# Optimization experiments

Hardware: AMD Instinct MI355X
Metric: run time of the kernel (lower is better)

## Reference

```python
import jax, jax.numpy as jnp
import numpy as np
import math

B, L, D, H, FF = 2, 2048, 1024, 16, 4096
FACTOR = 5
EPS = 1e-5


def _ln(x, g, b):
    mu = jnp.mean(x, axis=-1, keepdims=True)
    var = jnp.mean((x - mu) ** 2, axis=-1, keepdims=True)
    return (x - mu) * jax.lax.rsqrt(var + EPS) * g + b


def setup_inputs() -> dict:
    key = jax.random.key(0)
    ks = jax.random.split(key, 16)
    s = D ** -0.5
    sample_k = min(FACTOR * int(np.ceil(np.log(L))), L)  # 40
    return {
        "x": jax.random.normal(ks[0], (B, L, D), jnp.float32),
        "Wq": jax.random.normal(ks[1], (D, D), jnp.float32) * s,
        "bq": jnp.zeros((D,), jnp.float32),
        "Wk": jax.random.normal(ks[2], (D, D), jnp.float32) * s,
        "bk": jnp.zeros((D,), jnp.float32),
        "Wv": jax.random.normal(ks[3], (D, D), jnp.float32) * s,
        "bv": jnp.zeros((D,), jnp.float32),
        "Wo": jax.random.normal(ks[4], (D, D), jnp.float32) * s,
        "bo": jnp.zeros((D,), jnp.float32),
        "ln1_g": jnp.ones((D,), jnp.float32),
        "ln1_b": jnp.zeros((D,), jnp.float32),
        "W1": jax.random.normal(ks[5], (D, FF), jnp.float32) * s,
        "b1": jnp.zeros((FF,), jnp.float32),
        "W2": jax.random.normal(ks[6], (FF, D), jnp.float32) * (FF ** -0.5),
        "b2": jnp.zeros((D,), jnp.float32),
        "ln2_g": jnp.ones((D,), jnp.float32),
        "ln2_b": jnp.zeros((D,), jnp.float32),
        "index_sample": jax.random.randint(ks[7], (L, sample_k), 0, L),
    }


def _prob_attn(Q, K, V, index_sample):
    # Q,K,V: [B,H,L,Dh]; Informer ProbAttention with mask_flag=True (causal).
    b, h, l, dh = Q.shape
    n_top = min(FACTOR * int(np.ceil(np.log(l))), l)
    # sampled scores: Q[l] . K[index_sample[l, s]]
    K_s = K[:, :, index_sample]                                  # [B,H,L,S,Dh]
    QKs = jnp.einsum("bhld,bhlsd->bhls", Q, K_s)                 # [B,H,L,S]
    M = QKs.max(-1) - QKs.sum(-1) / l                             # sparsity measure
    _, M_top = jax.lax.top_k(M, n_top)                            # [B,H,u]
    Q_red = jnp.take_along_axis(Q, M_top[..., None], axis=2)      # [B,H,u,Dh]
    scale = 1.0 / jnp.sqrt(jnp.asarray(dh, jnp.float32))
    scores = jnp.einsum("bhud,bhld->bhul", Q_red, K) * scale      # [B,H,u,L]
    causal = jnp.arange(l)[None, None, None, :] > M_top[..., None]
    scores = jnp.where(causal, -jnp.inf, scores)
    attn = jax.nn.softmax(scores, axis=-1)
    upd = jnp.einsum("bhul,bhld->bhud", attn, V)                  # [B,H,u,Dh]
    # initial context for masked case: running cumsum of V
    context = jnp.cumsum(V, axis=2)
    bi = jnp.arange(b)[:, None, None]
    hi = jnp.arange(h)[None, :, None]
    context = context.at[bi, hi, M_top].set(upd)
    return context                                               # [B,H,L,Dh]


def reference(x, Wq, bq, Wk, bk, Wv, bv, Wo, bo, ln1_g, ln1_b,
              W1, b1, W2, b2, ln2_g, ln2_b, index_sample):
    b, l, d = x.shape
    dh = d // H
    Q = (x @ Wq + bq).reshape(b, l, H, dh).transpose(0, 2, 1, 3)
    K = (x @ Wk + bk).reshape(b, l, H, dh).transpose(0, 2, 1, 3)
    V = (x @ Wv + bv).reshape(b, l, H, dh).transpose(0, 2, 1, 3)
    ctx = _prob_attn(Q, K, V, index_sample)
    ctx = ctx.transpose(0, 2, 1, 3).reshape(b, l, d)
    attn_out = ctx @ Wo + bo
    x1 = _ln(x + attn_out, ln1_g, ln1_b)
    ff = jnp.maximum(x1 @ W1 + b1, 0.0) @ W2 + b2
    return _ln(x1 + ff, ln2_g, ln2_b)
```

## Files before the change

kernel.cpp:

```cpp
#include <hip/hip_runtime.h>
#include <hip/hip_bf16.h>
#include <hip/hip_fp16.h>
#include <math.h>

constexpr int B = 2, L = 2048, D = 1024, H = 16, DH = 64, FFD = 4096;
constexpr int S = 40;
constexpr int U = 40;
constexpr float EPS = 1e-5f;
constexpr int NCHUNK = 32;
constexpr int CHLEN = L / NCHUNK;
constexpr int LD3 = 3 * D;
constexpr int LD2 = 2 * D;
constexpr int LDA2 = 2 * D;
constexpr int JT = 128;
constexpr int NJC = L / JT;

typedef __attribute__((ext_vector_type(8))) short short8;
typedef __attribute__((ext_vector_type(8))) _Float16 half8;
typedef __attribute__((ext_vector_type(4))) float f32x4;

__device__ __forceinline__ unsigned short f2bf(float v) {
  __hip_bfloat16 h = __float2bfloat16(v);
  return __builtin_bit_cast(unsigned short, h);
}
__device__ __forceinline__ float bf2f(unsigned short u) {
  unsigned int x = ((unsigned int)u) << 16;
  return __builtin_bit_cast(float, x);
}
__device__ __forceinline__ unsigned short f2h(float v) {
  __half h = __float2half(v);
  return __builtin_bit_cast(unsigned short, h);
}
__device__ __forceinline__ float h2f(unsigned short u) {
  return __half2float(__builtin_bit_cast(__half, u));
}

__device__ __forceinline__ void gload16(const void* g, void* l) {
  __builtin_amdgcn_global_load_lds(
      (const __attribute__((address_space(1))) void*)g,
      (__attribute__((address_space(3))) void*)l, 16, 0, 0);
}

template<int GBN, int MINB, bool RELU, bool OUT_BF16, bool F16, bool DUPA>
__global__ __launch_bounds__(256, MINB) void gemm_kernel(
    const unsigned short* __restrict__ A,
    const unsigned short* __restrict__ Bt,
    const float* __restrict__ bias,
    const float* __restrict__ biasB,
    void* __restrict__ C, int M, int N, int K, int KA) {
  constexpr int GBM = 128, GBK = 64;
  constexpr int ABUF = GBM * GBK;
  constexpr int BBUF = GBN * GBK;
  constexpr int BUFS = ABUF + BBUF;
  constexpr int NI = GBN / 32;
  constexpr int NLOADS = 4 + GBN / 32;
  __shared__ short lds[2 * BUFS];

  const int tid  = threadIdx.x;
  const int lane = tid & 63;
  const int wid  = tid >> 6;
  const int wr = wid >> 1;
  const int wc = wid & 1;

  const int nwg  = gridDim.x * gridDim.y;
  const int orig = blockIdx.y * gridDim.x + blockIdx.x;
  const int wg   = (orig & 7) * (nwg >> 3) + (orig >> 3);
  const int bm = (wg / gridDim.x) * GBM;
  const int bn = (wg % gridDim.x) * GBN;

  const int srow  = lane >> 3;
  const int sslot = (lane & 7) ^ srow;
  const unsigned short* aS = A  + (size_t)(bm + wid * 8 + srow) * KA + sslot * 8;
  const unsigned short* bS = Bt + (size_t)(bn + wid * 8 + srow) * K  + sslot * 8;
  short* la0 = lds + wid * 8 * GBK;
  short* lb0 = lds + ABUF + wid * 8 * GBK;

  auto STAGE = [&](int buf, int kt) {
    const int akt = (DUPA && kt >= 16) ? kt - 16 : kt;
    const unsigned short* ap = aS + (size_t)akt * GBK;
    const unsigned short* bp = bS + (size_t)kt  * GBK;
    short* la = la0 + buf * BUFS;
    short* lb = lb0 + buf * BUFS;
    gload16(ap,                   la);
    gload16(ap + (size_t)32 * KA, la + 32 * GBK);
    gload16(ap + (size_t)64 * KA, la + 64 * GBK);
    gload16(ap + (size_t)96 * KA, la + 96 * GBK);
    #pragma unroll
    for (int r = 0; r < GBN / 32; ++r)
      gload16(bp + (size_t)(r * 32) * K, lb + r * 32 * GBK);
  };

  const int fr = lane & 15, g = lane >> 4;
  const int nt = K / GBK;

  STAGE(0, 0);

  f32x4 acc[4][NI] = {};
  int cur = 0;
  for (int t = 0; t < nt; ++t) {
    const int kt = (t + 1 < nt) ? t + 1 : t;
    STAGE(cur ^ 1, kt);
    if constexpr (NLOADS == 8)
      asm volatile("s_waitcnt vmcnt(8)" ::: "memory");
    else
      asm volatile("s_waitcnt vmcnt(6)" ::: "memory");
    __builtin_amdgcn_sched_barrier(0);
    __builtin_amdgcn_s_barrier();

    const short* la = lds + cur * BUFS;
    const short* lb = la + ABUF;
    short8 av[2][4], bv[2][NI];
    #pragma unroll
    for (int kk = 0; kk < 2; ++kk) {
      #pragma unroll
      for (int mi = 0; mi < 4; ++mi) {
        const int row = wr * 64 + mi * 16 + fr;
        av[kk][mi] = *(const short8*)&la[row * GBK + ((((kk << 2) | g) ^ (fr & 7)) << 3)];
      }
      #pragma unroll
      for (int ni = 0; ni < NI; ++ni) {
        const int row = wc * (GBN / 2) + ni * 16 + fr;
        bv[kk][ni] = *(const short8*)&lb[row * GBK + ((((kk << 2) | g) ^ (fr & 7)) << 3)];
      }
    }
    __builtin_amdgcn_s_setprio(1);
    #pragma unroll
    for (int kk = 0; kk < 2; ++kk)
      #pragma unroll
      for (int mi = 0; mi < 4; ++mi)
        #pragma unroll
        for (int ni = 0; ni < NI; ++ni) {
          if constexpr (F16)
            acc[mi][ni] = __builtin_amdgcn_mfma_f32_16x16x32_f16(
                __builtin_bit_cast(half8, av[kk][mi]),
                __builtin_bit_cast(half8, bv[kk][ni]), acc[mi][ni], 0, 0, 0);
          else
            acc[mi][ni] = __builtin_amdgcn_mfma_f32_16x16x32_bf16(
                av[kk][mi], bv[kk][ni], acc[mi][ni], 0, 0, 0);
        }
    __builtin_amdgcn_s_setprio(0);
    asm volatile("s_waitcnt lgkmcnt(0)" ::: "memory");
    __builtin_amdgcn_sched_barrier(0);
    __builtin_amdgcn_s_barrier();
    cur ^= 1;
  }

  #pragma unroll
  for (int ni = 0; ni < NI; ++ni) {
    const int col = bn + wc * (GBN / 2) + ni * 16 + fr;
    const float bcol = DUPA ? (col < D ? bias[col] : biasB[col - D]) : bias[col];
    #pragma unroll
    for (int mi = 0; mi < 4; ++mi) {
      #pragma unroll
      for (int j = 0; j < 4; ++j) {
        const int rowg = bm + wr * 64 + mi * 16 + (g << 2) + j;
        float v = acc[mi][ni][j] + bcol;
        if (RELU) v = fmaxf(v, 0.f);
        if (OUT_BF16) ((unsigned short*)C)[(size_t)rowg * N + col] = f2bf(v);
        else          ((float*)C)[(size_t)rowg * N + col] = v;
      }
    }
  }
}

__global__ __launch_bounds__(256) void split_x_f16_kernel(
    const float* __restrict__ x, unsigned short* __restrict__ A2,
    unsigned short* __restrict__ xb) {
  const int i = (blockIdx.x * 256 + threadIdx.x) * 4;
  if (i >= B * L * D) return;
  const int m = i / D, k = i % D;
  const float4 v = *(const float4*)(x + i);
  ushort4 hi, lo, bb;
  hi.x = f2h(v.x); lo.x = f2h(v.x - h2f(hi.x)); bb.x = f2bf(v.x);
  hi.y = f2h(v.y); lo.y = f2h(v.y - h2f(hi.y)); bb.y = f2bf(v.y);
  hi.z = f2h(v.z); lo.z = f2h(v.z - h2f(hi.z)); bb.z = f2bf(v.z);
  hi.w = f2h(v.w); lo.w = f2h(v.w - h2f(hi.w)); bb.w = f2bf(v.w);
  unsigned short* row = A2 + (size_t)m * LDA2;
  *(ushort4*)(row + k)     = hi;
  *(ushort4*)(row + D + k) = lo;
  *(ushort4*)(xb + i) = bb;
}

__global__ __launch_bounds__(256) void wsplit_f16_kernel(
    const float* __restrict__ W, unsigned short* __restrict__ B2r) {
  __shared__ float tile[32][33];
  const int bx = blockIdx.x * 32;
  const int by = blockIdx.y * 32;
  const int tx = threadIdx.x & 31, ty = threadIdx.x >> 5;
  #pragma unroll
  for (int i = ty; i < 32; i += 8)
    tile[i][tx] = W[(size_t)(by + i) * D + bx + tx];
  __syncthreads();
  #pragma unroll
  for (int i = ty; i < 32; i += 8) {
    const float v = tile[tx][i];
    const unsigned short hi = f2h(v);
    const unsigned short lo = f2h(v - h2f(hi));
    unsigned short* r = B2r + (size_t)(bx + i) * LD3 + (by + tx);
    r[0]     = hi;
    r[D]     = lo;
    r[2 * D] = hi;
  }
}

__global__ __launch_bounds__(256) void transpose4_bf16_kernel(
    const float* __restrict__ Wv, const float* __restrict__ Wo,
    const float* __restrict__ W1, const float* __restrict__ W2,
    unsigned short* __restrict__ Wvt, unsigned short* __restrict__ Wot,
    unsigned short* __restrict__ W1t, unsigned short* __restrict__ W2t) {
  const int bid = blockIdx.x;
  const float* W; unsigned short* Wt; int K, N, t;
  if (bid < 1024)      { W = Wv; Wt = Wvt; K = D;   N = D;   t = bid; }
  else if (bid < 2048) { W = Wo; Wt = Wot; K = D;   N = D;   t = bid - 1024; }
  else if (bid < 6144) { W = W1; Wt = W1t; K = D;   N = FFD; t = bid - 2048; }
  else                 { W = W2; Wt = W2t; K = FFD; N = D;   t = bid - 6144; }
  const int nx = N / 32;
  const int bx = (t % nx) * 32;
  const int by = (t / nx) * 32;
  __shared__ float tile[32][33];
  const int tx = threadIdx.x & 31, ty = threadIdx.x >> 5;
  #pragma unroll
  for (int i = ty; i < 32; i += 8)
    tile[i][tx] = W[(size_t)(by + i) * N + bx + tx];
  __syncthreads();
  #pragma unroll
  for (int i = ty; i < 32; i += 8)
    Wt[(size_t)(bx + i) * K + by + tx] = f2bf(tile[tx][i]);
}

__global__ __launch_bounds__(256) void prob_m_kernel(
    const float* __restrict__ QK, const int* __restrict__ idx,
    float* __restrict__ M_) {
  const int combo = blockIdx.x;
  const int b = combo >> 2, hg = combo & 3;
  const int l = blockIdx.y;
  const int tid = threadIdx.x;
  const int wave = tid >> 6;
  const int lane = tid & 63;
  const int h = hg * 4 + wave;
  __shared__ int sidx[S];
  if (tid < S) sidx[tid] = idx[l * S + tid];
  __syncthreads();
  const int dsub = (lane & 15) * 4;
  const int sgrp = lane >> 4;
  const float4 q = *(const float4*)(QK + ((size_t)b * L + l) * LD2 + h * DH + dsub);
  float mx = -INFINITY, sm = 0.f;
  for (int s = sgrp; s < S; s += 4) {
    const float4 kv = *(const float4*)(QK + ((size_t)b * L + sidx[s]) * LD2 + D + h * DH + dsub);
    float p = q.x*kv.x + q.y*kv.y + q.z*kv.z + q.w*kv.w;
    p += __shfl_xor(p, 1);
    p += __shfl_xor(p, 2);
    p += __shfl_xor(p, 4);
    p += __shfl_xor(p, 8);
    mx = fmaxf(mx, p);
    sm += p;
  }
  mx = fmaxf(mx, __shfl_xor(mx, 16));
  mx = fmaxf(mx, __shfl_xor(mx, 32));
  sm += __shfl_xor(sm, 16);
  sm += __shfl_xor(sm, 32);
  if (lane == 0)
    M_[((size_t)b * H + h) * L + l] = mx - sm / (float)L;
}

__global__ __launch_bounds__(64) void topk_kernel(
    const float* __restrict__ M_, int* __restrict__ Mtop) {
  const int bh = blockIdx.x;
  const float* row = M_ + (size_t)bh * L;
  const int lane = threadIdx.x;
  float v[32];
  #pragma unroll
  for (int k = 0; k < 32; ++k) v[k] = row[k * 64 + lane];
  for (int u = 0; u < U; ++u) {
    float best = v[0]; int bk = 0;
    #pragma unroll
    for (int k = 1; k < 32; ++k)
      if (v[k] > best) { best = v[k]; bk = k; }
    int bidx = bk * 64 + lane;
    #pragma unroll
    for (int off = 1; off < 64; off <<= 1) {
      const float ov = __shfl_xor(best, off);
      const int   oi = __shfl_xor(bidx, off);
      if (ov > best || (ov == best && oi < bidx)) { best = ov; bidx = oi; }
    }
    if (lane == 0) Mtop[bh * U + u] = bidx;
    if ((bidx & 63) == lane) {
      const int kk = bidx >> 6;
      #pragma unroll
      for (int k = 0; k < 32; ++k) if (k == kk) v[k] = -INFINITY;
    }
  }
}

__global__ __launch_bounds__(320) void attn_p1_kernel(
    const float* __restrict__ QK, const float* __restrict__ V,
    const int* __restrict__ Mtop,
    float* __restrict__ pmax, float* __restrict__ psum, float* __restrict__ pv) {
  const int jc = blockIdx.x, h = blockIdx.y, b = blockIdx.z;
  const int bh = b * H + h;
  const int tid = threadIdx.x;
  const int j0 = jc * JT;
  __shared__ float Qs[U][68];
  __shared__ float KVs[JT][68];
  __shared__ unsigned short ws[U][JT];

  for (int i = tid; i < U * 16; i += 320) {
    const int u = i >> 4, dq = (i & 15) << 2;
    const int row = Mtop[bh * U + u];
    *(float4*)&Qs[u][dq] =
        *(const float4*)(QK + ((size_t)b * L + row) * LD2 + h * DH + dq);
  }
  for (int i = tid; i < JT * 16; i += 320) {
    const int j = i >> 4, dq = (i & 15) << 2;
    *(float4*)&KVs[j][dq] =
        *(const float4*)(QK + ((size_t)b * L + j0 + j) * LD2 + D + h * DH + dq);
  }
  __syncthreads();

  const int u = tid >> 3, jg = tid & 7;
  const int mt = Mtop[bh * U + u];
  float sc[16];
  #pragma unroll
  for (int jt = 0; jt < 16; ++jt) sc[jt] = 0.f;
  for (int dq = 0; dq < 64; dq += 4) {
    const float4 q = *(const float4*)&Qs[u][dq];
    #pragma unroll
    for (int jt = 0; jt < 16; ++jt) {
      const float4 k = *(const float4*)&KVs[jt * 8 + jg][dq];
      sc[jt] += q.x*k.x + q.y*k.y + q.z*k.z + q.w*k.w;
    }
  }
  float m = -INFINITY;
  #pragma unroll
  for (int jt = 0; jt < 16; ++jt) {
    const int j = j0 + jt * 8 + jg;
    sc[jt] = (j <= mt) ? sc[jt] * 0.125f : -INFINITY;
    m = fmaxf(m, sc[jt]);
  }
  m = fmaxf(m, __shfl_xor(m, 1));
  m = fmaxf(m, __shfl_xor(m, 2));
  m = fmaxf(m, __shfl_xor(m, 4));
  float sum = 0.f;
  #pragma unroll
  for (int jt = 0; jt < 16; ++jt) {
    const float e = (sc[jt] == -INFINITY) ? 0.f : expf(sc[jt] - m);
    sum += e;
    ws[u][jt * 8 + jg] = f2bf(e);
  }
  sum += __shfl_xor(sum, 1);
  sum += __shfl_xor(sum, 2);
  sum += __shfl_xor(sum, 4);
  if (jg == 0) {
    pmax[(size_t)(bh * NJC + jc) * U + u] = m;
    psum[(size_t)(bh * NJC + jc) * U + u] = sum;
  }
  __syncthreads();
  for (int i = tid; i < JT * 16; i += 320) {
    const int j = i >> 4, dq = (i & 15) << 2;
    *(float4*)&KVs[j][dq] =
        *(const float4*)(V + ((size_t)b * L + j0 + j) * D + h * DH + dq);
  }
  __syncthreads();
  const int d = tid & 63, ug = tid >> 6;
  float acc[8] = {};
  for (int j = 0; j < JT; j += 2) {
    const float v0 = KVs[j][d], v1 = KVs[j + 1][d];
    #pragma unroll
    for (int k = 0; k < 8; ++k) {
      const int uu = ug + k * 5;
      const unsigned int wp = *(const unsigned int*)&ws[uu][j];
      acc[k] = fmaf(bf2f((unsigned short)(wp & 0xffff)), v0, acc[k]);
      acc[k] = fmaf(bf2f((unsigned short)(wp >> 16)), v1, acc[k]);
    }
  }
  #pragma unroll
  for (int k = 0; k < 8; ++k) {
    const int uu = ug + k * 5;
    pv[((size_t)(bh * NJC + jc) * U + uu) * DH + d] = acc[k];
  }
}

__global__ __launch_bounds__(64) void attn_p2_kernel(
    const float* __restrict__ pmax, const float* __restrict__ psum,
    const float* __restrict__ pv, const int* __restrict__ Mtop,
    unsigned short* __restrict__ ctx16) {
  const int bid = blockIdx.x;
  const int u = bid % U, bh = bid / U;
  const int d = threadIdx.x;
  float gmax = -INFINITY;
  for (int c = 0; c < NJC; ++c)
    gmax = fmaxf(gmax, pmax[(size_t)(bh * NJC + c) * U + u]);
  float den = 0.f, num = 0.f;
  for (int c = 0; c < NJC; ++c) {
    const float m = pmax[(size_t)(bh * NJC + c) * U + u];
    if (m == -INFINITY) continue;
    const float s = expf(m - gmax);
    den += psum[(size_t)(bh * NJC + c) * U + u] * s;
    num += pv[((size_t)(bh * NJC + c) * U + u) * DH + d] * s;
  }
  const int h = bh % H, b = bh / H;
  const int l = Mtop[bh * U + u];
  ctx16[((size_t)b * L + l) * D + h * DH + d] = f2bf(num / den);
}

__global__ __launch_bounds__(256) void cumsum_pass1(
    const float* __restrict__ V, float* __restrict__ ctx, float* __restrict__ csums) {
  const int c = blockIdx.x * 256 + threadIdx.x;
  const int ch = blockIdx.y, b = blockIdx.z;
  size_t base = ((size_t)b * L + (size_t)ch * CHLEN) * D + c;
  float acc = 0.f;
  for (int i = 0; i < CHLEN; ++i) {
    const size_t o = base + (size_t)i * D;
    acc += V[o];
    ctx[o] = acc;
  }
  csums[((size_t)b * NCHUNK + ch) * D + c] = acc;
}

__global__ __launch_bounds__(256) void cumsum_pass2(
    const float* __restrict__ ctx, const float* __restrict__ csums,
    unsigned short* __restrict__ ctx16) {
  const int c = blockIdx.x * 256 + threadIdx.x;
  const int ch = blockIdx.y, b = blockIdx.z;
  float off = 0.f;
  for (int j = 0; j < ch; ++j) off += csums[((size_t)b * NCHUNK + j) * D + c];
  size_t base = ((size_t)b * L + (size_t)ch * CHLEN) * D + c;
  for (int i = 0; i < CHLEN; ++i) {
    const size_t o = base + (size_t)i * D;
    ctx16[o] = f2bf(ctx[o] + off);
  }
}

template<bool ABF16>
__global__ __launch_bounds__(256) void add_ln_kernel(
    const void* __restrict__ a_, const float* __restrict__ r,
    const float* __restrict__ g, const float* __restrict__ be,
    float* __restrict__ out, unsigned short* __restrict__ out16) {
  const int row = blockIdx.x;
  const int tid = threadIdx.x;
  __shared__ float buf[D];
  __shared__ float red[256];
  const float* pr = r + (size_t)row * D;
  float s = 0.f;
  for (int i = tid; i < D; i += 256) {
    float av;
    if (ABF16) av = bf2f(((const unsigned short*)a_)[(size_t)row * D + i]);
    else       av = ((const float*)a_)[(size_t)row * D + i];
    float v = av + pr[i];
    buf[i] = v; s += v;
  }
  red[tid] = s; __syncthreads();
  for (int off = 128; off > 0; off >>= 1) {
    if (tid < off) red[tid] += red[tid+off];
    __syncthreads();
  }
  const float mu = red[0] / (float)D;
  __syncthreads();
  float s2 = 0.f;
  for (int i = tid; i < D; i += 256) { float dv = buf[i] - mu; s2 += dv * dv; }
  red[tid] = s2; __syncthreads();
  for (int off = 128; off > 0; off >>= 1) {
    if (tid < off) red[tid] += red[tid+off];
    __syncthreads();
  }
  const float rstd = rsqrtf(red[0] / (float)D + EPS);
  __syncthreads();
  for (int i = tid; i < D; i += 256) {
    float v = (buf[i] - mu) * rstd * g[i] + be[i];
    if (out)   out[(size_t)row * D + i] = v;
    if (out16) out16[(size_t)row * D + i] = f2bf(v);
  }
}

extern "C" void kernel_launch(void* const* d_in, const int* in_sizes, int n_in,
                              void* d_out, int out_size, void* d_ws, size_t ws_size,
                              hipStream_t stream) {
  const float* x   = (const float*)d_in[0];
  const float* Wq  = (const float*)d_in[1];
  const float* bq  = (const float*)d_in[2];
  const float* Wk  = (const float*)d_in[3];
  const float* bk  = (const float*)d_in[4];
  const float* Wv  = (const float*)d_in[5];
  const float* bv  = (const float*)d_in[6];
  const float* Wo  = (const float*)d_in[7];
  const float* bo  = (const float*)d_in[8];
  const float* g1  = (const float*)d_in[9];
  const float* be1 = (const float*)d_in[10];
  const float* W1  = (const float*)d_in[11];
  const float* b1  = (const float*)d_in[12];
  const float* W2  = (const float*)d_in[13];
  const float* b2  = (const float*)d_in[14];
  const float* g2  = (const float*)d_in[15];
  const float* be2 = (const float*)d_in[16];
  const int*   idx = (const int*)d_in[17];
  float* out = (float*)d_out;

  char* p = (char*)d_ws;
  unsigned short* A2   = (unsigned short*)p;
  float*          ctxb = (float*)p;
  float*          AO   = (float*)p;
  float*          ff2  = (float*)p;
  unsigned short* xb    = (unsigned short*)(p + 16777216);
  unsigned short* ctx16 = (unsigned short*)(p + 16777216);
  unsigned short* B2 = (unsigned short*)(p + 25165824);
  char* scr = p + 25165824;
  float* Mbuf   = (float*)(scr);
  float* csum   = (float*)(scr + 262144);
  int*   Mtop   = (int*)  (scr + 524288);
  float* pmax   = (float*)(scr + 532480);
  float* psum   = (float*)(scr + 614400);
  float* pv     = (float*)(scr + 696320);
  float*          QKb = (float*)(p + 37748736);
  unsigned short* x1b = (unsigned short*)(p + 54525952);
  unsigned short* ff1b = (unsigned short*)(p + 62914560);
  float* Vb = (float*)(p + 96468992);
  unsigned short* Wvt = (unsigned short*)(p + 113246208);
  unsigned short* Wot = (unsigned short*)(p + 115343360);
  unsigned short* W1t = (unsigned short*)(p + 117440512);
  unsigned short* W2t = (unsigned short*)(p + 125829120);

  dim3 blk(256);
  const int M = B * L;
  const int SZ = B * L * D;

  split_x_f16_kernel<<<(SZ/4 + 255)/256, blk, 0, stream>>>(x, A2, xb);
  wsplit_f16_kernel<<<dim3(D/32, D/32), blk, 0, stream>>>(Wq, B2);
  wsplit_f16_kernel<<<dim3(D/32, D/32), blk, 0, stream>>>(Wk, B2 + (size_t)D * LD3);
  gemm_kernel<128,2,false,false,true,true><<<dim3(LD2/128, M/128), blk, 0, stream>>>(
      A2, B2, bq, bk, QKb, M, LD2, LD3, LDA2);
  transpose4_bf16_kernel<<<10240, blk, 0, stream>>>(Wv, Wo, W1, W2, Wvt, Wot, W1t, W2t);
  gemm_kernel<64,3,false,false,false,false><<<dim3(D/64, M/128), blk, 0, stream>>>(
      xb, Wvt, bv, bv, Vb, M, D, D, D);
  prob_m_kernel<<<dim3(8, L), blk, 0, stream>>>(QKb, idx, Mbuf);
  topk_kernel<<<B*H, dim3(64), 0, stream>>>(Mbuf, Mtop);
  attn_p1_kernel<<<dim3(NJC, H, B), dim3(320), 0, stream>>>(QKb, Vb, Mtop, pmax, psum, pv);
  cumsum_pass1<<<dim3(D/256, NCHUNK, B), blk, 0, stream>>>(Vb, ctxb, csum);
  cumsum_pass2<<<dim3(D/256, NCHUNK, B), blk, 0, stream>>>(ctxb, csum, ctx16);
  attn_p2_kernel<<<B*H*U, dim3(64), 0, stream>>>(pmax, psum, pv, Mtop, ctx16);
  gemm_kernel<64,3,false,false,false,false><<<dim3(D/64, M/128), blk, 0, stream>>>(
      ctx16, Wot, bo, bo, AO, M, D, D, D);
  add_ln_kernel<false><<<B*L, blk, 0, stream>>>(x, AO, g1, be1, nullptr, x1b);
  gemm_kernel<128,2,true,true,false,false><<<dim3(FFD/128, M/128), blk, 0, stream>>>(
      x1b, W1t, b1, b1, ff1b, M, FFD, D, D);
  gemm_kernel<64,3,false,false,false,false><<<dim3(D/64, M/128), blk, 0, stream>>>(
      ff1b, W2t, b2, b2, ff2, M, D, FFD, FFD);
  add_ln_kernel<true><<<B*L, blk, 0, stream>>>(x1b, ff2, g2, be2, out,
                                               (unsigned short*)nullptr);
}
```

Baseline: 366.8 us.

## Store V, attention output and FFN output as bf16; restructure cumsum to avoid fp32 scratch

The V, Wo and W2 GEMMs now write bf16 outputs instead of fp32. Attention, cumsum and the add+LayerNorm kernels are adapted to read bf16. The cumsum no longer writes an intermediate fp32 prefix buffer: pass1 only computes chunk sums and pass2 recomputes the prefix from V directly, with two columns per thread. The two Wq/Wk split launches are merged into one grid. This cuts memory traffic and launches, at the cost of reduced precision in V, the residual branches, and the cumulative-sum context.

```diff
diff --git a/kernel.cpp b/kernel.cpp
--- a/kernel.cpp
+++ b/kernel.cpp
@@ -182,7 +182,10 @@
 }
 
 __global__ __launch_bounds__(256) void wsplit_f16_kernel(
-    const float* __restrict__ W, unsigned short* __restrict__ B2r) {
+    const float* __restrict__ Wq, const float* __restrict__ Wk,
+    unsigned short* __restrict__ B2r) {
+  const float* W = blockIdx.z ? Wk : Wq;
+  unsigned short* outb = B2r + (size_t)blockIdx.z * D * LD3;
   __shared__ float tile[32][33];
   const int bx = blockIdx.x * 32;
   const int by = blockIdx.y * 32;
@@ -196,7 +199,7 @@
     const float v = tile[tx][i];
     const unsigned short hi = f2h(v);
     const unsigned short lo = f2h(v - h2f(hi));
-    unsigned short* r = B2r + (size_t)(bx + i) * LD3 + (by + tx);
+    unsigned short* r = outb + (size_t)(bx + i) * LD3 + (by + tx);
     r[0]     = hi;
     r[D]     = lo;
     r[2 * D] = hi;
@@ -293,7 +296,7 @@
 }
 
 __global__ __launch_bounds__(320) void attn_p1_kernel(
-    const float* __restrict__ QK, const float* __restrict__ V,
+    const float* __restrict__ QK, const unsigned short* __restrict__ V16,
     const int* __restrict__ Mtop,
     float* __restrict__ pmax, float* __restrict__ psum, float* __restrict__ pv) {
   const int jc = blockIdx.x, h = blockIdx.y, b = blockIdx.z;
@@ -355,10 +358,12 @@
     psum[(size_t)(bh * NJC + jc) * U + u] = sum;
   }
   __syncthreads();
-  for (int i = tid; i < JT * 16; i += 320) {
-    const int j = i >> 4, dq = (i & 15) << 2;
-    *(float4*)&KVs[j][dq] =
-        *(const float4*)(V + ((size_t)b * L + j0 + j) * D + h * DH + dq);
+  for (int i = tid; i < JT * 8; i += 320) {
+    const int j = i >> 3, d8 = (i & 7) << 3;
+    short8 vv = *(const short8*)(V16 + ((size_t)b * L + j0 + j) * D + h * DH + d8);
+    #pragma unroll
+    for (int e = 0; e < 8; ++e)
+      KVs[j][d8 + e] = bf2f((unsigned short)vv[e]);
   }
   __syncthreads();
   const int d = tid & 63, ug = tid >> 6;
@@ -404,49 +409,56 @@
 }
 
 __global__ __launch_bounds__(256) void cumsum_pass1(
-    const float* __restrict__ V, float* __restrict__ ctx, float* __restrict__ csums) {
-  const int c = blockIdx.x * 256 + threadIdx.x;
+    const unsigned short* __restrict__ V16, float* __restrict__ csums) {
+  const int cp = blockIdx.x * 256 + threadIdx.x;
   const int ch = blockIdx.y, b = blockIdx.z;
-  size_t base = ((size_t)b * L + (size_t)ch * CHLEN) * D + c;
-  float acc = 0.f;
+  size_t base = ((size_t)b * L + (size_t)ch * CHLEN) * D + cp * 2;
+  float a0 = 0.f, a1 = 0.f;
+  for (int i = 0; i < CHLEN; ++i) {
+    const unsigned int u = *(const unsigned int*)(V16 + base + (size_t)i * D);
+    a0 += bf2f((unsigned short)(u & 0xffff));
+    a1 += bf2f((unsigned short)(u >> 16));
+  }
+  float* cs = csums + ((size_t)b * NCHUNK + ch) * D + cp * 2;
+  cs[0] = a0; cs[1] = a1;
+}
+
+__global__ __launch_bounds__(256) void cumsum_pass2(
+    const unsigned short* __restrict__ V16, const float* __restrict__ csums,
+    unsigned short* __restrict__ ctx16) {
+  const int cp = blockIdx.x * 256 + threadIdx.x;
+  const int ch = blockIdx.y, b = blockIdx.z;
+  float a0 = 0.f, a1 = 0.f;
+  for (int j = 0; j < ch; ++j) {
+    const float* cs = csums + ((size_t)b * NCHUNK + j) * D + cp * 2;
+    a0 += cs[0]; a1 += cs[1];
+  }
+  size_t base = ((size_t)b * L + (size_t)ch * CHLEN) * D + cp * 2;
   for (int i = 0; i < CHLEN; ++i) {
     const size_t o = base + (size_t)i * D;
-    acc += V[o];
-    ctx[o] = acc;
-  }
-  csums[((size_t)b * NCHUNK + ch) * D + c] = acc;
-}
-
-__global__ __launch_bounds__(256) void cumsum_pass2(
-    const float* __restrict__ ctx, const float* __restrict__ csums,
-    unsigned short* __restrict__ ctx16) {
-  const int c = blockIdx.x * 256 + threadIdx.x;
-  const int ch = blockIdx.y, b = blockIdx.z;
-  float off = 0.f;
-  for (int j = 0; j < ch; ++j) off += csums[((size_t)b * NCHUNK + j) * D + c];
-  size_t base = ((size_t)b * L + (size_t)ch * CHLEN) * D + c;
-  for (int i = 0; i < CHLEN; ++i) {
-    const size_t o = base + (size_t)i * D;
-    ctx16[o] = f2bf(ctx[o] + off);
+    const unsigned int u = *(const unsigned int*)(V16 + o);
+    a0 += bf2f((unsigned short)(u & 0xffff));
+    a1 += bf2f((unsigned short)(u >> 16));
+    *(unsigned int*)(ctx16 + o) =
+        (unsigned int)f2bf(a0) | ((unsigned int)f2bf(a1) << 16);
   }
 }
 
 template<bool ABF16>
 __global__ __launch_bounds__(256) void add_ln_kernel(
-    const void* __restrict__ a_, const float* __restrict__ r,
+    const void* __restrict__ a_, const unsigned short* __restrict__ r,
     const float* __restrict__ g, const float* __restrict__ be,
     float* __restrict__ out, unsigned short* __restrict__ out16) {
   const int row = blockIdx.x;
   const int tid = threadIdx.x;
   __shared__ float buf[D];
   __shared__ float red[256];
-  const float* pr = r + (size_t)row * D;
   float s = 0.f;
   for (int i = tid; i < D; i += 256) {
     float av;
     if (ABF16) av = bf2f(((const unsigned short*)a_)[(size_t)row * D + i]);
     else       av = ((const float*)a_)[(size_t)row * D + i];
-    float v = av + pr[i];
+    float v = av + bf2f(r[(size_t)row * D + i]);
     buf[i] = v; s += v;
   }
   red[tid] = s; __syncthreads();
@@ -496,10 +508,9 @@
   float* out = (float*)d_out;
 
   char* p = (char*)d_ws;
-  unsigned short* A2   = (unsigned short*)p;
-  float*          ctxb = (float*)p;
-  float*          AO   = (float*)p;
-  float*          ff2  = (float*)p;
+  unsigned short* A2     = (unsigned short*)p;
+  unsigned short* AO16   = (unsigned short*)p;
+  unsigned short* ff2_16 = (unsigned short*)(p + 8388608);
   unsigned short* xb    = (unsigned short*)(p + 16777216);
   unsigned short* ctx16 = (unsigned short*)(p + 16777216);
   unsigned short* B2 = (unsigned short*)(p + 25165824);
@@ -513,7 +524,7 @@
   float*          QKb = (float*)(p + 37748736);
   unsigned short* x1b = (unsigned short*)(p + 54525952);
   unsigned short* ff1b = (unsigned short*)(p + 62914560);
-  float* Vb = (float*)(p + 96468992);
+  unsigned short* Vb16 = (unsigned short*)(p + 96468992);
   unsigned short* Wvt = (unsigned short*)(p + 113246208);
   unsigned short* Wot = (unsigned short*)(p + 115343360);
   unsigned short* W1t = (unsigned short*)(p + 117440512);
@@ -524,26 +535,25 @@
   const int SZ = B * L * D;
 
   split_x_f16_kernel<<<(SZ/4 + 255)/256, blk, 0, stream>>>(x, A2, xb);
-  wsplit_f16_kernel<<<dim3(D/32, D/32), blk, 0, stream>>>(Wq, B2);
-  wsplit_f16_kernel<<<dim3(D/32, D/32), blk, 0, stream>>>(Wk, B2 + (size_t)D * LD3);
+  wsplit_f16_kernel<<<dim3(D/32, D/32, 2), blk, 0, stream>>>(Wq, Wk, B2);
   gemm_kernel<128,2,false,false,true,true><<<dim3(LD2/128, M/128), blk, 0, stream>>>(
       A2, B2, bq, bk, QKb, M, LD2, LD3, LDA2);
   transpose4_bf16_kernel<<<10240, blk, 0, stream>>>(Wv, Wo, W1, W2, Wvt, Wot, W1t, W2t);
-  gemm_kernel<64,3,false,false,false,false><<<dim3(D/64, M/128), blk, 0, stream>>>(
-      xb, Wvt, bv, bv, Vb, M, D, D, D);
+  gemm_kernel<64,3,false,true,false,false><<<dim3(D/64, M/128), blk, 0, stream>>>(
+      xb, Wvt, bv, bv, Vb16, M, D, D, D);
   prob_m_kernel<<<dim3(8, L), blk, 0, stream>>>(QKb, idx, Mbuf);
   topk_kernel<<<B*H, dim3(64), 0, stream>>>(Mbuf, Mtop);
-  attn_p1_kernel<<<dim3(NJC, H, B), dim3(320), 0, stream>>>(QKb, Vb, Mtop, pmax, psum, pv);
-  cumsum_pass1<<<dim3(D/256, NCHUNK, B), blk, 0, stream>>>(Vb, ctxb, csum);
-  cumsum_pass2<<<dim3(D/256, NCHUNK, B), blk, 0, stream>>>(ctxb, csum, ctx16);
+  attn_p1_kernel<<<dim3(NJC, H, B), dim3(320), 0, stream>>>(QKb, Vb16, Mtop, pmax, psum, pv);
+  cumsum_pass1<<<dim3(D/512, NCHUNK, B), blk, 0, stream>>>(Vb16, csum);
+  cumsum_pass2<<<dim3(D/512, NCHUNK, B), blk, 0, stream>>>(Vb16, csum, ctx16);
   attn_p2_kernel<<<B*H*U, dim3(64), 0, stream>>>(pmax, psum, pv, Mtop, ctx16);
-  gemm_kernel<64,3,false,false,false,false><<<dim3(D/64, M/128), blk, 0, stream>>>(
-      ctx16, Wot, bo, bo, AO, M, D, D, D);
-  add_ln_kernel<false><<<B*L, blk, 0, stream>>>(x, AO, g1, be1, nullptr, x1b);
+  gemm_kernel<64,3,false,true,false,false><<<dim3(D/64, M/128), blk, 0, stream>>>(
+      ctx16, Wot, bo, bo, AO16, M, D, D, D);
+  add_ln_kernel<false><<<B*L, blk, 0, stream>>>(x, AO16, g1, be1, nullptr, x1b);
   gemm_kernel<128,2,true,true,false,false><<<dim3(FFD/128, M/128), blk, 0, stream>>>(
       x1b, W1t, b1, b1, ff1b, M, FFD, D, D);
-  gemm_kernel<64,3,false,false,false,false><<<dim3(D/64, M/128), blk, 0, stream>>>(
-      ff1b, W2t, b2, b2, ff2, M, D, FFD, FFD);
-  add_ln_kernel<true><<<B*L, blk, 0, stream>>>(x1b, ff2, g2, be2, out,
+  gemm_kernel<64,3,false,true,false,false><<<dim3(D/64, M/128), blk, 0, stream>>>(
+      ff1b, W2t, b2, b2, ff2_16, M, D, FFD, FFD);
+  add_ln_kernel<true><<<B*L, blk, 0, stream>>>(x1b, ff2_16, g2, be2, out,
                                                (unsigned short*)nullptr);
 }
```

Result: faster. 350.8 us (-4.4%).
